# Performance work log

Measured on AMD Instinct MI355X. Metric: run time of the kernel, lower is better.

The kernel has to match this reference:

```python
import jax, jax.numpy as jnp
import numpy as np

N_NODES = 50000
N_EDGES = 800000
IN_DIM = 128
HID = 128
MLP_DIMS = [512, 256]


def setup_inputs() -> dict:
    key = jax.random.key(0)
    ks = jax.random.split(key, 12)
    x = jax.random.normal(ks[0], (N_NODES, IN_DIM), dtype=jnp.float32)
    edge_index = jax.random.randint(ks[1], (2, N_EDGES), 0, N_NODES, dtype=jnp.int64)
    s = 1.0 / np.sqrt(HID)
    inp = {"x": x, "edge_index": edge_index}
    # 3 GCN layers: 128->128, 128->128, 128->128
    dims_in = [IN_DIM, HID, HID]
    for i, di in enumerate(dims_in):
        inp[f"Wg{i}"] = jax.random.normal(ks[2 + i], (di, HID), dtype=jnp.float32) * (1.0 / np.sqrt(di))
        inp[f"bg{i}"] = jnp.zeros((HID,), dtype=jnp.float32)
    # MLP head: 128->512->256, ReLU after each Linear
    mlp_in = [HID, MLP_DIMS[0]]
    for i, (di, do) in enumerate(zip(mlp_in, MLP_DIMS)):
        inp[f"Wm{i}"] = jax.random.normal(ks[6 + i], (di, do), dtype=jnp.float32) * (1.0 / np.sqrt(di))
        inp[f"bm{i}"] = jnp.zeros((do,), dtype=jnp.float32)
    return inp


def _gcn_prep(edge_index, n):
    # add self-loops (PyG GCNConv default), compute symmetric normalization
    loops = jnp.arange(n, dtype=edge_index.dtype)
    src = jnp.concatenate([edge_index[0], loops])
    dst = jnp.concatenate([edge_index[1], loops])
    deg = jax.ops.segment_sum(jnp.ones_like(src, dtype=jnp.float32), dst, num_segments=n)
    dinv = jax.lax.rsqrt(deg)  # deg >= 1 due to self-loops
    norm = dinv[src] * dinv[dst]  # [E+N]
    return src, dst, norm


def _gcn_layer(x, W, b, src, dst, norm, n):
    h = x @ W  # [N, HID]
    msg = h[src] * norm[:, None]  # gather + scale, [E+N, HID]
    out = jax.ops.segment_sum(msg, dst, num_segments=n)  # scatter-add
    return out + b


def reference(x, edge_index, Wg0, bg0, Wg1, bg1, Wg2, bg2, Wm0, bm0, Wm1, bm1):
    n = x.shape[0]
    src, dst, norm = _gcn_prep(edge_index, n)
    h = x
    for W, b in ((Wg0, bg0), (Wg1, bg1), (Wg2, bg2)):
        h = jax.nn.relu(_gcn_layer(h, W, b, src, dst, norm, n))
    # MLP head (ends with ReLU: pop() only removed the trailing Dropout)
    h = jax.nn.relu(h @ Wm0 + bm0)
    h = jax.nn.relu(h @ Wm1 + bm1)
    return h
```

## Files before the change

kernel.cpp:

```cpp
#include <hip/hip_runtime.h>

#define HID 128

typedef _Float16 half8 __attribute__((ext_vector_type(8)));
typedef _Float16 half4h __attribute__((ext_vector_type(4)));
using float4v = __attribute__((ext_vector_type(4))) float;

typedef const __attribute__((address_space(1))) unsigned int* gas_ptr;
typedef __attribute__((address_space(3))) unsigned int* las_ptr;
__device__ __forceinline__ void gld16(const void* g, void* l) {
    __builtin_amdgcn_global_load_lds((gas_ptr)g, (las_ptr)l, 16, 0, 0);
}


__global__ void deg_int_kernel(const int* __restrict__ dst, int* __restrict__ degi, int E) {
    int i = blockIdx.x * blockDim.x + threadIdx.x;
    if (i < E) atomicAdd(&degi[dst[i]], 1);
}

__global__ __launch_bounds__(1024) void scan1_kernel(
    const int* __restrict__ in, int* __restrict__ incl, int* __restrict__ bsums, int N) {
    __shared__ int sm[1024];
    int i = blockIdx.x * 1024 + threadIdx.x;
    int v = (i < N) ? in[i] : 0;
    sm[threadIdx.x] = v;
    __syncthreads();
    for (int off = 1; off < 1024; off <<= 1) {
        int t = (threadIdx.x >= (unsigned)off) ? sm[threadIdx.x - off] : 0;
        __syncthreads();
        sm[threadIdx.x] += t;
        __syncthreads();
    }
    if (i < N) incl[i] = sm[threadIdx.x];
    if (threadIdx.x == 1023) bsums[blockIdx.x] = sm[1023];
}

__global__ __launch_bounds__(1024) void scan2_kernel(int* __restrict__ bsums, int nblk) {
    __shared__ int sm[1024];
    int t = threadIdx.x;
    int v = (t < nblk) ? bsums[t] : 0;
    sm[t] = v;
    __syncthreads();
    for (int off = 1; off < 1024; off <<= 1) {
        int u = (t >= (unsigned)off) ? sm[t - off] : 0;
        __syncthreads();
        sm[t] += u;
        __syncthreads();
    }
    if (t < nblk) bsums[t] = sm[t] - v;
}

__global__ void scan3_kernel(const int* __restrict__ incl, const int* __restrict__ degi,
                             const int* __restrict__ bsums, int* __restrict__ rowptr,
                             int* __restrict__ cursor, float* __restrict__ dinv, int N, int E) {
    int i = blockIdx.x * blockDim.x + threadIdx.x;
    if (i < N) {
        int r = bsums[i >> 10] + incl[i] - degi[i];
        rowptr[i] = r;
        cursor[i] = r;
        dinv[i] = rsqrtf((float)degi[i] + 1.0f);
    }
    if (i == 0) rowptr[N] = E;
}

__global__ void fill_kernel(const int* __restrict__ src, const int* __restrict__ dst,
                            int* __restrict__ cursor, int* __restrict__ col, int E) {
    int e = blockIdx.x * blockDim.x + threadIdx.x;
    if (e < E) {
        int d = dst[e];
        int pos = atomicAdd(&cursor[d], 1);
        col[pos] = src[e];
    }
}


__global__ void xconv_kernel(const float* __restrict__ x, _Float16* __restrict__ Xh, int total4) {
    int i = blockIdx.x * blockDim.x + threadIdx.x;
    if (i >= total4) return;
    const float4 v = *(const float4*)(x + (size_t)i * 4);
    half4h h;
    h.x = (_Float16)v.x; h.y = (_Float16)v.y; h.z = (_Float16)v.z; h.w = (_Float16)v.w;
    *(half4h*)(Xh + (size_t)i * 4) = h;
}

struct WSegs {
    const float* W[5];
    _Float16* H[5];
    int K[5], M[5], start[5];
};

__global__ void wconv_all_kernel(WSegs S, int total) {
    int idx = blockIdx.x * blockDim.x + threadIdx.x;
    if (idx >= total) return;
    int s = 0;
#pragma unroll
    for (int t = 1; t < 5; ++t)
        if (idx >= S.start[t]) s = t;
    int local = idx - S.start[s];
    int M = S.M[s], K = S.K[s];
    int k = local / M;
    int m = local - k * M;
    S.H[s][(size_t)m * K + k] = (_Float16)S.W[s][local];
}

__global__ __launch_bounds__(256) void gather_kernel(
    const _Float16* __restrict__ hs, const int* __restrict__ rowptr,
    const int* __restrict__ col, const float* __restrict__ dinv,
    const float* __restrict__ bias, _Float16* __restrict__ Ch, int N) {
    long long idx = (long long)blockIdx.x * blockDim.x + threadIdx.x;
    int i = (int)(idx >> 5);
    if (i >= N) return;
    int c = ((int)idx & 31) * 4;

    int beg = rowptr[i];
    int end = rowptr[i + 1];

    const half4h sv = *(const half4h*)(hs + (size_t)i * HID + c);
    float ax = (float)sv.x, ay = (float)sv.y, az = (float)sv.z, aw = (float)sv.w;

    int j = beg;
    for (; j + 4 <= end; j += 4) {
        int s0 = col[j], s1 = col[j + 1], s2 = col[j + 2], s3 = col[j + 3];
        const half4h v0 = *(const half4h*)(hs + (size_t)s0 * HID + c);
        const half4h v1 = *(const half4h*)(hs + (size_t)s1 * HID + c);
        const half4h v2 = *(const half4h*)(hs + (size_t)s2 * HID + c);
        const half4h v3 = *(const half4h*)(hs + (size_t)s3 * HID + c);
        ax += (float)v0.x + (float)v1.x + (float)v2.x + (float)v3.x;
        ay += (float)v0.y + (float)v1.y + (float)v2.y + (float)v3.y;
        az += (float)v0.z + (float)v1.z + (float)v2.z + (float)v3.z;
        aw += (float)v0.w + (float)v1.w + (float)v2.w + (float)v3.w;
    }
    for (; j < end; ++j) {
        int s = col[j];
        const half4h v = *(const half4h*)(hs + (size_t)s * HID + c);
        ax += (float)v.x; ay += (float)v.y; az += (float)v.z; aw += (float)v.w;
    }

    float di = dinv[i];
    float4 b = *(const float4*)(bias + c);
    half4h r;
    r.x = (_Float16)fmaxf(ax * di + b.x, 0.0f);
    r.y = (_Float16)fmaxf(ay * di + b.y, 0.0f);
    r.z = (_Float16)fmaxf(az * di + b.z, 0.0f);
    r.w = (_Float16)fmaxf(aw * di + b.w, 0.0f);
    *(half4h*)(Ch + (size_t)i * HID + c) = r;
}

template <bool SCALE, bool BIAS, bool RELU, bool OUTHALF>
__global__ __launch_bounds__(256, 4) void gemm2h(
    const _Float16* __restrict__ Ah, const _Float16* __restrict__ Bh,
    const float* __restrict__ bias, const float* __restrict__ rowscale,
    float* __restrict__ outF, _Float16* __restrict__ outH, int Nout, int K, int M) {
    __shared__ _Float16 lds[2 * 6144];

    const int tid = threadIdx.x;
    const int bm = blockIdx.y * 64;
    const int bn = blockIdx.x * 128;
    const int wave = tid >> 6, lane = tid & 63;
    const int quad = lane >> 4, c16 = lane & 15;
    const int wn = wave * 32;

    float4v acc[4][2];
#pragma unroll
    for (int a = 0; a < 4; ++a)
#pragma unroll
        for (int b = 0; b < 2; ++b)
#pragma unroll
            for (int r = 0; r < 4; ++r) acc[a][b][r] = 0.0f;

    const int r0 = tid >> 2;
    const int kq0 = (tid & 3) * 8;

    const _Float16* gA  = Ah + (size_t)(bm + r0) * K + kq0;
    const _Float16* gB0 = Bh + (size_t)(bn + r0) * K + kq0;
    const _Float16* gB1 = Bh + (size_t)(bn + r0 + 64) * K + kq0;

    auto issue = [&](int c) {
        _Float16* buf = lds + (size_t)(c & 1) * 6144;
        int k0 = c * 32;
        gld16(gA + k0, buf + (size_t)tid * 8);
        gld16(gB0 + k0, buf + 2048 + (size_t)tid * 8);
        gld16(gB1 + k0, buf + 2048 + (size_t)(tid + 256) * 8);
    };

    issue(0);
    __syncthreads();

    const int nch = K >> 5;
    for (int c = 0; c < nch; ++c) {
        if (c + 1 < nch) issue(c + 1);

        const _Float16* buf = lds + (size_t)(c & 1) * 6144;
        half8 af[4], bf[2];
#pragma unroll
        for (int t = 0; t < 4; ++t)
            af[t] = *(const half8*)&buf[(t * 16 + c16) * 32 + quad * 8];
#pragma unroll
        for (int t = 0; t < 2; ++t)
            bf[t] = *(const half8*)&buf[2048 + (wn + t * 16 + c16) * 32 + quad * 8];
#pragma unroll
        for (int tm = 0; tm < 4; ++tm)
#pragma unroll
            for (int tn = 0; tn < 2; ++tn)
                acc[tm][tn] = __builtin_amdgcn_mfma_f32_16x16x32_f16(af[tm], bf[tn], acc[tm][tn], 0, 0, 0);
        __syncthreads();
    }

#pragma unroll
    for (int tm = 0; tm < 4; ++tm) {
#pragma unroll
        for (int tn = 0; tn < 2; ++tn) {
            int colg = bn + wn + tn * 16 + c16;
            float bv = BIAS ? bias[colg] : 0.0f;
#pragma unroll
            for (int r = 0; r < 4; ++r) {
                int row = bm + tm * 16 + quad * 4 + r;
                if (row >= Nout) continue;
                float v = acc[tm][tn][r];
                if (SCALE) v *= rowscale[row];
                if (BIAS) v += bv;
                if (RELU) v = fmaxf(v, 0.0f);
                if (OUTHALF) outH[(size_t)row * M + colg] = (_Float16)v;
                else         outF[(size_t)row * M + colg] = v;
            }
        }
    }
}


extern "C" void kernel_launch(void* const* d_in, const int* in_sizes, int n_in,
                              void* d_out, int out_size, void* d_ws, size_t ws_size,
                              hipStream_t stream) {
    const float* x   = (const float*)d_in[0];
    const int*   ei  = (const int*)d_in[1];
    const float* Wg0 = (const float*)d_in[2];
    const float* bg0 = (const float*)d_in[3];
    const float* Wg1 = (const float*)d_in[4];
    const float* bg1 = (const float*)d_in[5];
    const float* Wg2 = (const float*)d_in[6];
    const float* bg2 = (const float*)d_in[7];
    const float* Wm0 = (const float*)d_in[8];
    const float* bm0 = (const float*)d_in[9];
    const float* Wm1 = (const float*)d_in[10];
    const float* bm1 = (const float*)d_in[11];
    float* out = (float*)d_out;

    const int N  = in_sizes[0] / HID;
    const int E  = in_sizes[1] / 2;
    const int M0 = in_sizes[9];
    const int M1 = in_sizes[11];
    const int Npad = ((N + 127) / 128) * 128;
    const int nblk1024 = (N + 1023) / 1024;

    const int* src = ei;
    const int* dst = ei + E;

    char* ws = (char*)d_ws;
    size_t off = 0;
    auto alloc = [&](size_t bytes) {
        void* p = ws + off;
        off += (bytes + 255) & ~(size_t)255;
        return p;
    };
    int* degi   = (int*)alloc((size_t)N * 4);
    int* tmp    = (int*)alloc((size_t)N * 4);
    int* bsums  = (int*)alloc(4096);
    int* rowptr = (int*)alloc((size_t)(N + 1) * 4);
    int* cursor = (int*)alloc((size_t)N * 4);
    int* colbuf = (int*)alloc((size_t)E * 4);
    float* dinv = (float*)alloc((size_t)N * 4);
    _Float16* WgT[3];
    for (int l = 0; l < 3; ++l)
        WgT[l] = (_Float16*)alloc((size_t)HID * HID * 2);
    _Float16* Wm0T = (_Float16*)alloc((size_t)M0 * HID * 2);
    _Float16* Wm1T = (_Float16*)alloc((size_t)M1 * M0 * 2);
    _Float16* Xh = (_Float16*)alloc((size_t)Npad * HID * 2);
    _Float16* Hs = (_Float16*)alloc((size_t)Npad * HID * 2);
    _Float16* Ch = (_Float16*)alloc((size_t)Npad * HID * 2);
    _Float16* Mh = (_Float16*)alloc((size_t)Npad * M0 * 2);

    hipMemsetAsync(degi, 0, (size_t)N * 4, stream);
    deg_int_kernel<<<(E + 255) / 256, 256, 0, stream>>>(dst, degi, E);
    scan1_kernel<<<nblk1024, 1024, 0, stream>>>(degi, tmp, bsums, N);
    scan2_kernel<<<1, 1024, 0, stream>>>(bsums, nblk1024);
    scan3_kernel<<<(N + 255) / 256, 256, 0, stream>>>(tmp, degi, bsums, rowptr, cursor, dinv, N, E);
    fill_kernel<<<(E + 255) / 256, 256, 0, stream>>>(src, dst, cursor, colbuf, E);

    xconv_kernel<<<(N * HID / 4 + 255) / 256, 256, 0, stream>>>(x, Xh, N * HID / 4);
    {
        WSegs S;
        const float* Ws[5] = {Wg0, Wg1, Wg2, Wm0, Wm1};
        _Float16* Hs5[5]   = {WgT[0], WgT[1], WgT[2], Wm0T, Wm1T};
        int Ks[5] = {HID, HID, HID, HID, M0};
        int Ms[5] = {HID, HID, HID, M0, M1};
        int start = 0;
        for (int s = 0; s < 5; ++s) {
            S.W[s] = Ws[s]; S.H[s] = Hs5[s];
            S.K[s] = Ks[s]; S.M[s] = Ms[s]; S.start[s] = start;
            start += Ks[s] * Ms[s];
        }
        wconv_all_kernel<<<(start + 255) / 256, 256, 0, stream>>>(S, start);
    }

    const float* bg[3] = {bg0, bg1, bg2};
    const _Float16* cur = Xh;
    long long gatherThreads = (long long)N * 32;
    for (int l = 0; l < 3; ++l) {
        gemm2h<true, false, false, true><<<dim3(1, Npad / 64), 256, 0, stream>>>(
            cur, WgT[l], nullptr, dinv, nullptr, Hs, N, HID, HID);
        gather_kernel<<<(int)((gatherThreads + 255) / 256), 256, 0, stream>>>(
            Hs, rowptr, colbuf, dinv, bg[l], Ch, N);
        cur = Ch;
    }

    gemm2h<false, true, true, true><<<dim3(M0 / 128, Npad / 64), 256, 0, stream>>>(
        Ch, Wm0T, bm0, nullptr, nullptr, Mh, N, HID, M0);
    gemm2h<false, true, true, false><<<dim3(M1 / 128, Npad / 64), 256, 0, stream>>>(
        Mh, Wm1T, bm1, nullptr, out, nullptr, N, M0, M1);
}
```

Baseline: 398.0 us.

## Fuse preprocessing kernels, replace scan with wave-atomic offsets, widen gather to half8

Merges degree counting, x conversion and weight conversion into one multi-role launch. It replaces the three-kernel block scan with a per-wave shuffle scan that gets its base from a global atomic, which yields non-monotone but valid row begin/end arrays. The CSR fill is co-launched with the first layer GEMM, and the gather now uses 16 lanes with 8-wide half loads per node. The aim is fewer launches and serial dependencies, at the cost of nondeterministic row ordering and some GEMM blocks sharing the grid with atomic-heavy fill blocks.

```diff
diff --git a/kernel.cpp b/kernel.cpp
--- a/kernel.cpp
+++ b/kernel.cpp
@@ -10,77 +10,6 @@
 typedef __attribute__((address_space(3))) unsigned int* las_ptr;
 __device__ __forceinline__ void gld16(const void* g, void* l) {
     __builtin_amdgcn_global_load_lds((gas_ptr)g, (las_ptr)l, 16, 0, 0);
-}
-
-
-__global__ void deg_int_kernel(const int* __restrict__ dst, int* __restrict__ degi, int E) {
-    int i = blockIdx.x * blockDim.x + threadIdx.x;
-    if (i < E) atomicAdd(&degi[dst[i]], 1);
-}
-
-__global__ __launch_bounds__(1024) void scan1_kernel(
-    const int* __restrict__ in, int* __restrict__ incl, int* __restrict__ bsums, int N) {
-    __shared__ int sm[1024];
-    int i = blockIdx.x * 1024 + threadIdx.x;
-    int v = (i < N) ? in[i] : 0;
-    sm[threadIdx.x] = v;
-    __syncthreads();
-    for (int off = 1; off < 1024; off <<= 1) {
-        int t = (threadIdx.x >= (unsigned)off) ? sm[threadIdx.x - off] : 0;
-        __syncthreads();
-        sm[threadIdx.x] += t;
-        __syncthreads();
-    }
-    if (i < N) incl[i] = sm[threadIdx.x];
-    if (threadIdx.x == 1023) bsums[blockIdx.x] = sm[1023];
-}
-
-__global__ __launch_bounds__(1024) void scan2_kernel(int* __restrict__ bsums, int nblk) {
-    __shared__ int sm[1024];
-    int t = threadIdx.x;
-    int v = (t < nblk) ? bsums[t] : 0;
-    sm[t] = v;
-    __syncthreads();
-    for (int off = 1; off < 1024; off <<= 1) {
-        int u = (t >= (unsigned)off) ? sm[t - off] : 0;
-        __syncthreads();
-        sm[t] += u;
-        __syncthreads();
-    }
-    if (t < nblk) bsums[t] = sm[t] - v;
-}
-
-__global__ void scan3_kernel(const int* __restrict__ incl, const int* __restrict__ degi,
-                             const int* __restrict__ bsums, int* __restrict__ rowptr,
-                             int* __restrict__ cursor, float* __restrict__ dinv, int N, int E) {
-    int i = blockIdx.x * blockDim.x + threadIdx.x;
-    if (i < N) {
-        int r = bsums[i >> 10] + incl[i] - degi[i];
-        rowptr[i] = r;
-        cursor[i] = r;
-        dinv[i] = rsqrtf((float)degi[i] + 1.0f);
-    }
-    if (i == 0) rowptr[N] = E;
-}
-
-__global__ void fill_kernel(const int* __restrict__ src, const int* __restrict__ dst,
-                            int* __restrict__ cursor, int* __restrict__ col, int E) {
-    int e = blockIdx.x * blockDim.x + threadIdx.x;
-    if (e < E) {
-        int d = dst[e];
-        int pos = atomicAdd(&cursor[d], 1);
-        col[pos] = src[e];
-    }
-}
-
-
-__global__ void xconv_kernel(const float* __restrict__ x, _Float16* __restrict__ Xh, int total4) {
-    int i = blockIdx.x * blockDim.x + threadIdx.x;
-    if (i >= total4) return;
-    const float4 v = *(const float4*)(x + (size_t)i * 4);
-    half4h h;
-    h.x = (_Float16)v.x; h.y = (_Float16)v.y; h.z = (_Float16)v.z; h.w = (_Float16)v.w;
-    *(half4h*)(Xh + (size_t)i * 4) = h;
 }
 
 struct WSegs {
@@ -89,73 +18,70 @@
     int K[5], M[5], start[5];
 };
 
-__global__ void wconv_all_kernel(WSegs S, int total) {
-    int idx = blockIdx.x * blockDim.x + threadIdx.x;
-    if (idx >= total) return;
-    int s = 0;
-#pragma unroll
-    for (int t = 1; t < 5; ++t)
-        if (idx >= S.start[t]) s = t;
-    int local = idx - S.start[s];
-    int M = S.M[s], K = S.K[s];
-    int k = local / M;
-    int m = local - k * M;
-    S.H[s][(size_t)m * K + k] = (_Float16)S.W[s][local];
-}
-
-__global__ __launch_bounds__(256) void gather_kernel(
-    const _Float16* __restrict__ hs, const int* __restrict__ rowptr,
-    const int* __restrict__ col, const float* __restrict__ dinv,
-    const float* __restrict__ bias, _Float16* __restrict__ Ch, int N) {
-    long long idx = (long long)blockIdx.x * blockDim.x + threadIdx.x;
-    int i = (int)(idx >> 5);
-    if (i >= N) return;
-    int c = ((int)idx & 31) * 4;
-
-    int beg = rowptr[i];
-    int end = rowptr[i + 1];
-
-    const half4h sv = *(const half4h*)(hs + (size_t)i * HID + c);
-    float ax = (float)sv.x, ay = (float)sv.y, az = (float)sv.z, aw = (float)sv.w;
-
-    int j = beg;
-    for (; j + 4 <= end; j += 4) {
-        int s0 = col[j], s1 = col[j + 1], s2 = col[j + 2], s3 = col[j + 3];
-        const half4h v0 = *(const half4h*)(hs + (size_t)s0 * HID + c);
-        const half4h v1 = *(const half4h*)(hs + (size_t)s1 * HID + c);
-        const half4h v2 = *(const half4h*)(hs + (size_t)s2 * HID + c);
-        const half4h v3 = *(const half4h*)(hs + (size_t)s3 * HID + c);
-        ax += (float)v0.x + (float)v1.x + (float)v2.x + (float)v3.x;
-        ay += (float)v0.y + (float)v1.y + (float)v2.y + (float)v3.y;
-        az += (float)v0.z + (float)v1.z + (float)v2.z + (float)v3.z;
-        aw += (float)v0.w + (float)v1.w + (float)v2.w + (float)v3.w;
-    }
-    for (; j < end; ++j) {
-        int s = col[j];
-        const half4h v = *(const half4h*)(hs + (size_t)s * HID + c);
-        ax += (float)v.x; ay += (float)v.y; az += (float)v.z; aw += (float)v.w;
-    }
-
-    float di = dinv[i];
-    float4 b = *(const float4*)(bias + c);
-    half4h r;
-    r.x = (_Float16)fmaxf(ax * di + b.x, 0.0f);
-    r.y = (_Float16)fmaxf(ay * di + b.y, 0.0f);
-    r.z = (_Float16)fmaxf(az * di + b.z, 0.0f);
-    r.w = (_Float16)fmaxf(aw * di + b.w, 0.0f);
-    *(half4h*)(Ch + (size_t)i * HID + c) = r;
+__global__ __launch_bounds__(256) void fused_prep1(
+    const int* __restrict__ dst, int* __restrict__ degi, int E, int nDeg,
+    const float* __restrict__ x, _Float16* __restrict__ Xh, int total4, int nX,
+    WSegs S, int totalW) {
+    int bx = blockIdx.x;
+    if (bx < nDeg) {
+        int i = bx * 256 + (int)threadIdx.x;
+        if (i < E) atomicAdd(&degi[dst[i]], 1);
+    } else if (bx < nDeg + nX) {
+        int i = (bx - nDeg) * 256 + (int)threadIdx.x;
+        if (i >= total4) return;
+        const float4 v = *(const float4*)(x + (size_t)i * 4);
+        half4h h;
+        h.x = (_Float16)v.x; h.y = (_Float16)v.y; h.z = (_Float16)v.z; h.w = (_Float16)v.w;
+        *(half4h*)(Xh + (size_t)i * 4) = h;
+    } else {
+        int idx = (bx - nDeg - nX) * 256 + (int)threadIdx.x;
+        if (idx >= totalW) return;
+        int s = 0;
+#pragma unroll
+        for (int t = 1; t < 5; ++t)
+            if (idx >= S.start[t]) s = t;
+        int local = idx - S.start[s];
+        int M = S.M[s], K = S.K[s];
+        int k = local / M;
+        int m = local - k * M;
+        S.H[s][(size_t)m * K + k] = (_Float16)S.W[s][local];
+    }
+}
+
+__global__ __launch_bounds__(256) void prep2_kernel(
+    const int* __restrict__ degi, int* __restrict__ rowbeg, int* __restrict__ rowend,
+    int* __restrict__ cursor, float* __restrict__ dinv, int* __restrict__ tot, int N) {
+    int i = blockIdx.x * 256 + (int)threadIdx.x;
+    int lane = (int)threadIdx.x & 63;
+    int d = (i < N) ? degi[i] : 0;
+    int incl = d;
+#pragma unroll
+    for (int off = 1; off < 64; off <<= 1) {
+        int t = __shfl_up(incl, off, 64);
+        if (lane >= off) incl += t;
+    }
+    int wsum = __shfl(incl, 63, 64);
+    int wbase = 0;
+    if (lane == 63) wbase = atomicAdd(tot, wsum);
+    wbase = __shfl(wbase, 63, 64);
+    if (i < N) {
+        int b = wbase + incl - d;
+        rowbeg[i] = b;
+        rowend[i] = b + d;
+        cursor[i] = b;
+        dinv[i] = rsqrtf((float)d + 1.0f);
+    }
 }
 
 template <bool SCALE, bool BIAS, bool RELU, bool OUTHALF>
-__global__ __launch_bounds__(256, 4) void gemm2h(
-    const _Float16* __restrict__ Ah, const _Float16* __restrict__ Bh,
+__device__ __forceinline__ void gemm_body(
+    int bxc, int byr, const _Float16* __restrict__ Ah, const _Float16* __restrict__ Bh,
     const float* __restrict__ bias, const float* __restrict__ rowscale,
-    float* __restrict__ outF, _Float16* __restrict__ outH, int Nout, int K, int M) {
-    __shared__ _Float16 lds[2 * 6144];
-
+    float* __restrict__ outF, _Float16* __restrict__ outH, int Nout, int K, int M,
+    _Float16* lds) {
     const int tid = threadIdx.x;
-    const int bm = blockIdx.y * 64;
-    const int bn = blockIdx.x * 128;
+    const int bm = byr * 64;
+    const int bn = bxc * 128;
     const int wave = tid >> 6, lane = tid & 63;
     const int quad = lane >> 4, c16 = lane & 15;
     const int wn = wave * 32;
@@ -225,6 +151,81 @@
             }
         }
     }
+}
+
+template <bool SCALE, bool BIAS, bool RELU, bool OUTHALF>
+__global__ __launch_bounds__(256, 4) void gemm_std(
+    const _Float16* __restrict__ Ah, const _Float16* __restrict__ Bh,
+    const float* __restrict__ bias, const float* __restrict__ rowscale,
+    float* __restrict__ outF, _Float16* __restrict__ outH, int Nout, int K, int M) {
+    __shared__ _Float16 lds[2 * 6144];
+    gemm_body<SCALE, BIAS, RELU, OUTHALF>(blockIdx.x, blockIdx.y, Ah, Bh, bias, rowscale,
+                                          outF, outH, Nout, K, M, lds);
+}
+
+__global__ __launch_bounds__(256, 4) void fill_gemm_kernel(
+    const int* __restrict__ src, const int* __restrict__ dst,
+    int* __restrict__ cursor, int* __restrict__ col, int E, int nFill,
+    const _Float16* __restrict__ Ah, const _Float16* __restrict__ Bh,
+    const float* __restrict__ rowscale, _Float16* __restrict__ outH,
+    int Nout, int K, int M) {
+    __shared__ _Float16 lds[2 * 6144];
+    int bx = blockIdx.x;
+    if (bx < nFill) {
+        int e = bx * 256 + (int)threadIdx.x;
+        if (e < E) {
+            int d = dst[e];
+            int pos = atomicAdd(&cursor[d], 1);
+            col[pos] = src[e];
+        }
+    } else {
+        gemm_body<true, false, false, true>(0, bx - nFill, Ah, Bh, nullptr, rowscale,
+                                            nullptr, outH, Nout, K, M, lds);
+    }
+}
+
+__global__ __launch_bounds__(256) void gather_kernel(
+    const _Float16* __restrict__ hs, const int* __restrict__ rowbeg,
+    const int* __restrict__ rowend, const int* __restrict__ col,
+    const float* __restrict__ dinv, const float* __restrict__ bias,
+    _Float16* __restrict__ Ch, int N) {
+    long long idx = (long long)blockIdx.x * blockDim.x + threadIdx.x;
+    int i = (int)(idx >> 4);
+    if (i >= N) return;
+    int c = ((int)idx & 15) * 8;
+
+    int beg = rowbeg[i];
+    int end = rowend[i];
+
+    const half8 sv = *(const half8*)(hs + (size_t)i * HID + c);
+    float ax[8];
+#pragma unroll
+    for (int r = 0; r < 8; ++r) ax[r] = (float)sv[r];
+
+    int j = beg;
+    for (; j + 4 <= end; j += 4) {
+        int s0 = col[j], s1 = col[j + 1], s2 = col[j + 2], s3 = col[j + 3];
+        const half8 v0 = *(const half8*)(hs + (size_t)s0 * HID + c);
+        const half8 v1 = *(const half8*)(hs + (size_t)s1 * HID + c);
+        const half8 v2 = *(const half8*)(hs + (size_t)s2 * HID + c);
+        const half8 v3 = *(const half8*)(hs + (size_t)s3 * HID + c);
+#pragma unroll
+        for (int r = 0; r < 8; ++r)
+            ax[r] += ((float)v0[r] + (float)v1[r]) + ((float)v2[r] + (float)v3[r]);
+    }
+    for (; j < end; ++j) {
+        int s = col[j];
+        const half8 v = *(const half8*)(hs + (size_t)s * HID + c);
+#pragma unroll
+        for (int r = 0; r < 8; ++r) ax[r] += (float)v[r];
+    }
+
+    float di = dinv[i];
+    half8 rr;
+#pragma unroll
+    for (int r = 0; r < 8; ++r)
+        rr[r] = (_Float16)fmaxf(ax[r] * di + bias[c + r], 0.0f);
+    *(half8*)(Ch + (size_t)i * HID + c) = rr;
 }
 
 
@@ -250,7 +251,6 @@
     const int M0 = in_sizes[9];
     const int M1 = in_sizes[11];
     const int Npad = ((N + 127) / 128) * 128;
-    const int nblk1024 = (N + 1023) / 1024;
 
     const int* src = ei;
     const int* dst = ei + E;
@@ -263,9 +263,9 @@
         return p;
     };
     int* degi   = (int*)alloc((size_t)N * 4);
-    int* tmp    = (int*)alloc((size_t)N * 4);
-    int* bsums  = (int*)alloc(4096);
-    int* rowptr = (int*)alloc((size_t)(N + 1) * 4);
+    int* tot    = (int*)alloc(256);
+    int* rowbeg = (int*)alloc((size_t)N * 4);
+    int* rowend = (int*)alloc((size_t)N * 4);
     int* cursor = (int*)alloc((size_t)N * 4);
     int* colbuf = (int*)alloc((size_t)E * 4);
     float* dinv = (float*)alloc((size_t)N * 4);
@@ -279,16 +279,14 @@
     _Float16* Ch = (_Float16*)alloc((size_t)Npad * HID * 2);
     _Float16* Mh = (_Float16*)alloc((size_t)Npad * M0 * 2);
 
-    hipMemsetAsync(degi, 0, (size_t)N * 4, stream);
-    deg_int_kernel<<<(E + 255) / 256, 256, 0, stream>>>(dst, degi, E);
-    scan1_kernel<<<nblk1024, 1024, 0, stream>>>(degi, tmp, bsums, N);
-    scan2_kernel<<<1, 1024, 0, stream>>>(bsums, nblk1024);
-    scan3_kernel<<<(N + 255) / 256, 256, 0, stream>>>(tmp, degi, bsums, rowptr, cursor, dinv, N, E);
-    fill_kernel<<<(E + 255) / 256, 256, 0, stream>>>(src, dst, cursor, colbuf, E);
-
-    xconv_kernel<<<(N * HID / 4 + 255) / 256, 256, 0, stream>>>(x, Xh, N * HID / 4);
+    hipMemsetAsync(degi, 0, ((char*)tot - (char*)degi) + 256, stream);
+
+    const int nDeg = (E + 255) / 256;
+    const int total4 = N * HID / 4;
+    const int nX = (total4 + 255) / 256;
+    int totalW;
+    WSegs S;
     {
-        WSegs S;
         const float* Ws[5] = {Wg0, Wg1, Wg2, Wm0, Wm1};
         _Float16* Hs5[5]   = {WgT[0], WgT[1], WgT[2], Wm0T, Wm1T};
         int Ks[5] = {HID, HID, HID, HID, M0};
@@ -299,22 +297,33 @@
             S.K[s] = Ks[s]; S.M[s] = Ms[s]; S.start[s] = start;
             start += Ks[s] * Ms[s];
         }
-        wconv_all_kernel<<<(start + 255) / 256, 256, 0, stream>>>(S, start);
-    }
+        totalW = start;
+    }
+    const int nW = (totalW + 255) / 256;
+    fused_prep1<<<nDeg + nX + nW, 256, 0, stream>>>(
+        dst, degi, E, nDeg, x, Xh, total4, nX, S, totalW);
+
+    prep2_kernel<<<(N + 255) / 256, 256, 0, stream>>>(
+        degi, rowbeg, rowend, cursor, dinv, tot, N);
+
+    fill_gemm_kernel<<<nDeg + Npad / 64, 256, 0, stream>>>(
+        src, dst, cursor, colbuf, E, nDeg,
+        Xh, WgT[0], dinv, Hs, N, HID, HID);
 
     const float* bg[3] = {bg0, bg1, bg2};
-    const _Float16* cur = Xh;
-    long long gatherThreads = (long long)N * 32;
-    for (int l = 0; l < 3; ++l) {
-        gemm2h<true, false, false, true><<<dim3(1, Npad / 64), 256, 0, stream>>>(
-            cur, WgT[l], nullptr, dinv, nullptr, Hs, N, HID, HID);
-        gather_kernel<<<(int)((gatherThreads + 255) / 256), 256, 0, stream>>>(
-            Hs, rowptr, colbuf, dinv, bg[l], Ch, N);
-        cur = Ch;
-    }
-
-    gemm2h<false, true, true, true><<<dim3(M0 / 128, Npad / 64), 256, 0, stream>>>(
+    long long gatherThreads = (long long)N * 16;
+    int gblocks = (int)((gatherThreads + 255) / 256);
+    gather_kernel<<<gblocks, 256, 0, stream>>>(
+        Hs, rowbeg, rowend, colbuf, dinv, bg[0], Ch, N);
+    for (int l = 1; l < 3; ++l) {
+        gemm_std<true, false, false, true><<<dim3(1, Npad / 64), 256, 0, stream>>>(
+            Ch, WgT[l], nullptr, dinv, nullptr, Hs, N, HID, HID);
+        gather_kernel<<<gblocks, 256, 0, stream>>>(
+            Hs, rowbeg, rowend, colbuf, dinv, bg[l], Ch, N);
+    }
+
+    gemm_std<false, true, true, true><<<dim3(M0 / 128, Npad / 64), 256, 0, stream>>>(
         Ch, Wm0T, bm0, nullptr, nullptr, Mh, N, HID, M0);
-    gemm2h<false, true, true, false><<<dim3(M1 / 128, Npad / 64), 256, 0, stream>>>(
+    gemm_std<false, true, true, false><<<dim3(M1 / 128, Npad / 64), 256, 0, stream>>>(
         Mh, Wm1T, bm1, nullptr, out, nullptr, N, M0, M1);
 }
```

After: 397.6 us. About the same (-0.1%).
